# Optimization experiments

Hardware: AMD Instinct MI355X
Metric: run time of the kernel (lower is better)

The kernel has to match this reference:

```python
import jax, jax.numpy as jnp
import numpy as np

N, P = 65536, 1024

def setup_inputs() -> dict:
    key = jax.random.key(0)
    k1, k2, k3, k4 = jax.random.split(key, 4)
    X = jax.random.normal(k1, (N, P), dtype=jnp.float32)
    beta0 = jax.random.normal(k2, (1,), dtype=jnp.float32)
    beta = jax.random.normal(k3, (P,), dtype=jnp.float32)
    Theta = jax.random.normal(k4, (P, P), dtype=jnp.float32)
    return {"X": X, "beta0": beta0, "beta": beta, "Theta": Theta}

def reference(X, beta0, beta, Theta):
    # y_hat = beta0 + X @ beta + sum_{j<k} Theta[j,k] * X[:,j] * X[:,k]
    # The double loop uses only the strictly upper-triangular part of Theta.
    p = Theta.shape[0]
    theta_upper = jnp.triu(Theta, k=1)                     # [p, p]
    linear = beta0 + X @ beta                              # [n]
    interaction = jnp.sum((X @ theta_upper) * X, axis=1)   # [n], quadratic form
    return linear + interaction
```

## Files before the change

### kernel.cpp

```cpp
#include <hip/hip_runtime.h>


typedef __bf16 bf16_t;
typedef bf16_t bf16x8 __attribute__((ext_vector_type(8)));
typedef float f32x4 __attribute__((ext_vector_type(4)));
typedef unsigned short u16;
typedef u16 u16x4 __attribute__((ext_vector_type(4)));
typedef u16 u16x8 __attribute__((ext_vector_type(8)));

#define N_ROWS 65536
#define P_DIM  1024
#define BM 128
#define BN 128
#define BK 32

static __device__ __forceinline__ u16 f2bf(float f) {
  unsigned u = __builtin_bit_cast(unsigned, f);
  u += 0x7FFFu + ((u >> 16) & 1u);
  return (u16)(u >> 16);
}

static __device__ __forceinline__ void gload16(const void* g, void* lds_base) {
  __builtin_amdgcn_global_load_lds(
      (const __attribute__((address_space(1))) unsigned char*)g,
      (__attribute__((address_space(3))) unsigned char*)lds_base, 16, 0, 0);
}

__global__ void __launch_bounds__(256)
init_y(float* __restrict__ y, const float* __restrict__ beta0) {
  int i = blockIdx.x * blockDim.x + threadIdx.x;
  if (i < N_ROWS) y[i] = beta0[0];
}

__global__ void __launch_bounds__(128)
conv_theta(const float* __restrict__ Theta, u16* __restrict__ Tt,
           float* __restrict__ y, const float* __restrict__ beta0) {
  __shared__ float tile[32][33];
  const int tid = threadIdx.x;
  const int tg  = (blockIdx.y * gridDim.x + blockIdx.x) * 128 + tid;
  if (tg < N_ROWS) y[tg] = beta0[0];

  const int k0  = blockIdx.x * 32;
  const int c0  = blockIdx.y * 32;
  {
    const int tx = tid & 31;
    const int rb = tid >> 5;
    #pragma unroll
    for (int i = 0; i < 8; ++i) {
      int kl = rb * 8 + i;
      tile[kl][tx] = Theta[(size_t)(k0 + kl) * P_DIM + c0 + tx];
    }
  }
  __syncthreads();
  {
    const int cl = tid >> 2;
    const int qt = tid & 3;
    const int c  = c0 + cl;
    const int Q  = blockIdx.x * 4 + qt;
    u16x8 w;
    #pragma unroll
    for (int e = 0; e < 8; ++e) {
      int k = Q * 8 + e;
      float v = tile[qt * 8 + e][cl];
      w[e] = (k < c) ? f2bf(v) : (u16)0;
    }
    const int qs = (qt ^ ((c >> 1) & 3));
    *(u16x8*)(Tt + (size_t)c * P_DIM + (size_t)(blockIdx.x * 32 + qs * 8)) = w;
  }
}

__global__ void __launch_bounds__(512)
gemm_r13(const float* __restrict__ X, const u16* __restrict__ Tt,
         const float* __restrict__ beta, float* __restrict__ y)
{
  __shared__ __align__(16) u16 L[2][8192];

  const int nwg = (N_ROWS / BM) * (P_DIM / BN);
  const int swz = (blockIdx.x & 7) * (nwg / 8) + (blockIdx.x >> 3);
  const int bn  = 7 - (swz & 7);
  const int bm  = swz >> 3;
  const int c0  = bn * BN;
  const int m0  = bm * BM;
  const int nkt = (bn + 1) * 4;

  const int tid  = threadIdx.x;
  const int lane = tid & 63;
  const int wid  = tid >> 6;
  const int wm   = wid >> 1;
  const int wn   = wid & 1;
  const int l15  = lane & 15;
  const int lg   = lane >> 4;

  const int ar = tid >> 2;
  const int ap = tid & 3;
  const int aq = (ap ^ ((ar >> 1) & 3)) * 8;

  const int brow = wid * 16 + (lane >> 2);
  const int bq   = (lane & 3) * 8;

  f32x4 acc[2][4];
  #pragma unroll
  for (int i = 0; i < 2; ++i)
    #pragma unroll
    for (int j = 0; j < 4; ++j)
      acc[i][j] = (f32x4)0.0f;

  f32x4 av0, av1;

  #define STAGE_A_LOAD(t_)                                                      \
    {                                                                           \
      const float* s_ = X + (size_t)(m0 + ar) * P_DIM + (t_) * BK + ap * 8;     \
      av0 = ((const f32x4*)s_)[0];                                              \
      av1 = ((const f32x4*)s_)[1];                                              \
    }
  #define STAGE_A_WRITE(buf_)                                                   \
    {                                                                           \
      u16x8 w_;                                                                 \
      _Pragma("unroll")                                                         \
      for (int j = 0; j < 4; ++j) { w_[j] = f2bf(av0[j]); w_[j + 4] = f2bf(av1[j]); } \
      *(u16x8*)&L[buf_][ar * 32 + aq] = w_;                                     \
    }
  #define STAGE_B(buf_, t_)                                                     \
    gload16(Tt + (size_t)(c0 + brow) * P_DIM + (t_) * BK + bq,                  \
            &L[buf_][4096 + wid * 512]);

  STAGE_A_LOAD(0)
  STAGE_B(0, 0)
  asm volatile("s_waitcnt vmcnt(0)" ::: "memory");
  __builtin_amdgcn_sched_barrier(0);
  STAGE_A_WRITE(0)
  asm volatile("s_waitcnt lgkmcnt(0)" ::: "memory");
  __builtin_amdgcn_sched_barrier(0);
  __builtin_amdgcn_s_barrier();
  __builtin_amdgcn_sched_barrier(0);

  for (int t = 0; t < nkt; ++t) {
    const int cur = t & 1;
    const bool pre = (t + 1 < nkt);
    if (pre) { STAGE_A_LOAD(t + 1) STAGE_B(cur ^ 1, t + 1) }

    bf16x8 af[2], bfr[4];
    #pragma unroll
    for (int mi = 0; mi < 2; ++mi) {
      const int rw = wm * 32 + mi * 16 + l15;
      u16x8 v = *(const u16x8*)&L[cur][rw * 32 + (lg ^ ((rw >> 1) & 3)) * 8];
      af[mi] = __builtin_bit_cast(bf16x8, v);
    }
    #pragma unroll
    for (int ni = 0; ni < 4; ++ni) {
      const int cl = wn * 64 + ni * 16 + l15;
      u16x8 v = *(const u16x8*)&L[cur][4096 + cl * 32 + (lg ^ ((cl >> 1) & 3)) * 8];
      bfr[ni] = __builtin_bit_cast(bf16x8, v);
    }

    __builtin_amdgcn_s_setprio(1);
    #pragma unroll
    for (int mi = 0; mi < 2; ++mi)
      #pragma unroll
      for (int ni = 0; ni < 4; ++ni)
        acc[mi][ni] = __builtin_amdgcn_mfma_f32_16x16x32_bf16(bfr[ni], af[mi], acc[mi][ni], 0, 0, 0);
    __builtin_amdgcn_s_setprio(0);

    if (pre) {
      asm volatile("s_waitcnt vmcnt(0)" ::: "memory");
      __builtin_amdgcn_sched_barrier(0);
      STAGE_A_WRITE(cur ^ 1)
    }
    asm volatile("s_waitcnt lgkmcnt(0)" ::: "memory");
    __builtin_amdgcn_sched_barrier(0);
    __builtin_amdgcn_s_barrier();
    __builtin_amdgcn_sched_barrier(0);
  }
  #undef STAGE_A_LOAD
  #undef STAGE_A_WRITE
  #undef STAGE_B

  float ysum[2];
  ysum[0] = 0.0f; ysum[1] = 0.0f;

  #pragma unroll
  for (int mi = 0; mi < 2; ++mi) {
    const int row = m0 + wm * 32 + mi * 16 + l15;
    const float* xr = X + (size_t)row * P_DIM;
    #pragma unroll
    for (int ni = 0; ni < 4; ++ni) {
      const int cb = c0 + wn * 64 + ni * 16 + lg * 4;
      f32x4 xw = *(const f32x4*)(xr + cb);
      f32x4 bv = *(const f32x4*)(beta + cb);
      #pragma unroll
      for (int r = 0; r < 4; ++r)
        ysum[mi] += (acc[mi][ni][r] + bv[r]) * xw[r];
    }
  }

  #pragma unroll
  for (int mi = 0; mi < 2; ++mi) {
    ysum[mi] += __shfl_xor(ysum[mi], 16);
    ysum[mi] += __shfl_xor(ysum[mi], 32);
  }
  if (lane < 16) {
    #pragma unroll
    for (int mi = 0; mi < 2; ++mi)
      atomicAdd(&y[m0 + wm * 32 + mi * 16 + l15], ysum[mi]);
  }
}

#define LDT 40
__global__ void __launch_bounds__(256)
fused_quad_fallback(const float* __restrict__ X, const float* __restrict__ beta,
                    const float* __restrict__ Theta, float* __restrict__ y)
{
  __shared__ __align__(16) u16 Alds[128 * LDT];
  __shared__ __align__(16) u16 Blds[128 * LDT];

  const int bid = blockIdx.x;
  const int bn  = bid & 7;
  const int bm  = bid >> 3;
  const int c0  = bn * 128;
  const int m0  = bm * 128;
  const int nkt = (bn + 1) * 4;

  const int tid  = threadIdx.x;
  const int lane = tid & 63;
  const int wid  = tid >> 6;
  const int wm   = wid >> 1;
  const int wn   = wid & 1;
  const int l15  = lane & 15;
  const int lg   = lane >> 4;

  f32x4 acc[4][4];
  #pragma unroll
  for (int i = 0; i < 4; ++i)
    #pragma unroll
    for (int j = 0; j < 4; ++j)
      acc[i][j] = (f32x4)0.0f;

  const int arow  = tid >> 1;
  const int ahalf = (tid & 1) * 16;
  const int kb4 = (tid >> 5) * 4;
  const int cb4 = (tid & 31) * 4;

  for (int kt = 0; kt < nkt; ++kt) {
    const int k0 = kt * 32;
    __syncthreads();
    {
      const f32x4* p = (const f32x4*)(X + (size_t)(m0 + arow) * P_DIM + k0 + ahalf);
      f32x4 v0 = p[0], v1 = p[1], v2 = p[2], v3 = p[3];
      u16x8 w0, w1;
      #pragma unroll
      for (int i = 0; i < 4; ++i) {
        w0[i] = f2bf(v0[i]); w0[i + 4] = f2bf(v1[i]);
        w1[i] = f2bf(v2[i]); w1[i + 4] = f2bf(v3[i]);
      }
      *(u16x8*)&Alds[arow * LDT + ahalf]     = w0;
      *(u16x8*)&Alds[arow * LDT + ahalf + 8] = w1;
    }
    {
      float e[4][4];
      #pragma unroll
      for (int i = 0; i < 4; ++i) {
        f32x4 r = *(const f32x4*)(Theta + (size_t)(k0 + kb4 + i) * P_DIM + c0 + cb4);
        #pragma unroll
        for (int j = 0; j < 4; ++j)
          e[i][j] = ((k0 + kb4 + i) < (c0 + cb4 + j)) ? r[j] : 0.0f;
      }
      #pragma unroll
      for (int j = 0; j < 4; ++j) {
        u16x4 wv;
        #pragma unroll
        for (int i = 0; i < 4; ++i) wv[i] = f2bf(e[i][j]);
        *(u16x4*)&Blds[(cb4 + j) * LDT + kb4] = wv;
      }
    }
    __syncthreads();

    bf16x8 af[4], bfr[4];
    #pragma unroll
    for (int mi = 0; mi < 4; ++mi) {
      u16x8 t = *(const u16x8*)&Alds[(wm * 64 + mi * 16 + l15) * LDT + lg * 8];
      af[mi] = __builtin_bit_cast(bf16x8, t);
    }
    #pragma unroll
    for (int ni = 0; ni < 4; ++ni) {
      u16x8 t = *(const u16x8*)&Blds[(wn * 64 + ni * 16 + l15) * LDT + lg * 8];
      bfr[ni] = __builtin_bit_cast(bf16x8, t);
    }
    #pragma unroll
    for (int mi = 0; mi < 4; ++mi)
      #pragma unroll
      for (int ni = 0; ni < 4; ++ni)
        acc[mi][ni] = __builtin_amdgcn_mfma_f32_16x16x32_bf16(af[mi], bfr[ni], acc[mi][ni], 0, 0, 0);
  }

  float ysum[4][4];
  #pragma unroll
  for (int mi = 0; mi < 4; ++mi)
    #pragma unroll
    for (int r = 0; r < 4; ++r)
      ysum[mi][r] = 0.0f;

  #pragma unroll
  for (int ni = 0; ni < 4; ++ni) {
    const int col = c0 + wn * 64 + ni * 16 + l15;
    const float bta = beta[col];
    #pragma unroll
    for (int mi = 0; mi < 4; ++mi) {
      const int rowb = m0 + wm * 64 + mi * 16 + lg * 4;
      #pragma unroll
      for (int r = 0; r < 4; ++r) {
        float xv = X[(size_t)(rowb + r) * P_DIM + col];
        ysum[mi][r] += (acc[mi][ni][r] + bta) * xv;
      }
    }
  }

  #pragma unroll
  for (int m = 1; m < 16; m <<= 1)
    #pragma unroll
    for (int mi = 0; mi < 4; ++mi)
      #pragma unroll
      for (int r = 0; r < 4; ++r)
        ysum[mi][r] += __shfl_xor(ysum[mi][r], m);

  if (l15 == 0) {
    #pragma unroll
    for (int mi = 0; mi < 4; ++mi)
      #pragma unroll
      for (int r = 0; r < 4; ++r)
        atomicAdd(&y[m0 + wm * 64 + mi * 16 + lg * 4 + r], ysum[mi][r]);
  }
}

extern "C" void kernel_launch(void* const* d_in, const int* in_sizes, int n_in,
                              void* d_out, int out_size, void* d_ws, size_t ws_size,
                              hipStream_t stream) {
  const float* X     = (const float*)d_in[0];
  const float* beta0 = (const float*)d_in[1];
  const float* beta  = (const float*)d_in[2];
  const float* Theta = (const float*)d_in[3];
  float* y = (float*)d_out;

  const size_t need = (size_t)P_DIM * P_DIM * 2;
  if (ws_size >= need) {
    u16* Tt = (u16*)d_ws;
    conv_theta<<<dim3(32, 32), 128, 0, stream>>>(Theta, Tt, y, beta0);
    gemm_r13<<<(N_ROWS / BM) * (P_DIM / BN), 512, 0, stream>>>(X, Tt, beta, y);
  } else {
    init_y<<<N_ROWS / 256, 256, 0, stream>>>(y, beta0);
    fused_quad_fallback<<<(N_ROWS / 128) * (P_DIM / 128), 256, 0, stream>>>(X, beta, Theta, y);
  }
}
```

Baseline: 163.6 us.

## Triple-buffer Theta tiles to prefetch B two k-steps ahead

Splits LDS into a double buffer for the bf16-converted X tile and a triple buffer for the Theta tile loaded by global_load_lds. Theta tiles are now issued two iterations ahead while X stays one ahead, and the wait becomes vmcnt(2) so the newest B prefetch stays in flight across the barrier. The aim is to hide more global load latency for B. It costs extra LDS per block (40KB versus 32KB), which can reduce occupancy, and it depends on vmcnt ordering being correct.

```diff
diff --git a/kernel.cpp b/kernel.cpp
--- a/kernel.cpp
+++ b/kernel.cpp
@@ -70,10 +70,10 @@
 }
 
 __global__ void __launch_bounds__(512)
-gemm_r13(const float* __restrict__ X, const u16* __restrict__ Tt,
+gemm_r16(const float* __restrict__ X, const u16* __restrict__ Tt,
          const float* __restrict__ beta, float* __restrict__ y)
 {
-  __shared__ __align__(16) u16 L[2][8192];
+  __shared__ __align__(16) u16 L[20480];
 
   const int nwg = (N_ROWS / BM) * (P_DIM / BN);
   const int swz = (blockIdx.x & 7) * (nwg / 8) + (blockIdx.x >> 3);
@@ -113,19 +113,20 @@
       av0 = ((const f32x4*)s_)[0];                                              \
       av1 = ((const f32x4*)s_)[1];                                              \
     }
-  #define STAGE_A_WRITE(buf_)                                                   \
+  #define STAGE_A_WRITE(ab_)                                                    \
     {                                                                           \
       u16x8 w_;                                                                 \
       _Pragma("unroll")                                                         \
       for (int j = 0; j < 4; ++j) { w_[j] = f2bf(av0[j]); w_[j + 4] = f2bf(av1[j]); } \
-      *(u16x8*)&L[buf_][ar * 32 + aq] = w_;                                     \
-    }
-  #define STAGE_B(buf_, t_)                                                     \
+      *(u16x8*)&L[(ab_) * 4096 + ar * 32 + aq] = w_;                            \
+    }
+  #define STAGE_B(bb_, t_)                                                      \
     gload16(Tt + (size_t)(c0 + brow) * P_DIM + (t_) * BK + bq,                  \
-            &L[buf_][4096 + wid * 512]);
-
+            &L[8192 + (bb_) * 4096 + wid * 512]);
+
+  STAGE_B(0, 0)
+  STAGE_B(1, 1)
   STAGE_A_LOAD(0)
-  STAGE_B(0, 0)
   asm volatile("s_waitcnt vmcnt(0)" ::: "memory");
   __builtin_amdgcn_sched_barrier(0);
   STAGE_A_WRITE(0)
@@ -135,21 +136,24 @@
   __builtin_amdgcn_sched_barrier(0);
 
   for (int t = 0; t < nkt; ++t) {
-    const int cur = t & 1;
-    const bool pre = (t + 1 < nkt);
-    if (pre) { STAGE_A_LOAD(t + 1) STAGE_B(cur ^ 1, t + 1) }
+    const int acur = t & 1;
+    const int bcur = t % 3;
+    const bool pre1 = (t + 1 < nkt);
+    const bool pre2 = (t + 2 < nkt);
+    if (pre1) STAGE_A_LOAD(t + 1)
+    if (pre2) STAGE_B((t + 2) % 3, t + 2)
 
     bf16x8 af[2], bfr[4];
     #pragma unroll
     for (int mi = 0; mi < 2; ++mi) {
       const int rw = wm * 32 + mi * 16 + l15;
-      u16x8 v = *(const u16x8*)&L[cur][rw * 32 + (lg ^ ((rw >> 1) & 3)) * 8];
+      u16x8 v = *(const u16x8*)&L[acur * 4096 + rw * 32 + (lg ^ ((rw >> 1) & 3)) * 8];
       af[mi] = __builtin_bit_cast(bf16x8, v);
     }
     #pragma unroll
     for (int ni = 0; ni < 4; ++ni) {
       const int cl = wn * 64 + ni * 16 + l15;
-      u16x8 v = *(const u16x8*)&L[cur][4096 + cl * 32 + (lg ^ ((cl >> 1) & 3)) * 8];
+      u16x8 v = *(const u16x8*)&L[8192 + bcur * 4096 + cl * 32 + (lg ^ ((cl >> 1) & 3)) * 8];
       bfr[ni] = __builtin_bit_cast(bf16x8, v);
     }
 
@@ -161,11 +165,13 @@
         acc[mi][ni] = __builtin_amdgcn_mfma_f32_16x16x32_bf16(bfr[ni], af[mi], acc[mi][ni], 0, 0, 0);
     __builtin_amdgcn_s_setprio(0);
 
-    if (pre) {
+    if (pre2) {
+      asm volatile("s_waitcnt vmcnt(2)" ::: "memory");
+    } else {
       asm volatile("s_waitcnt vmcnt(0)" ::: "memory");
-      __builtin_amdgcn_sched_barrier(0);
-      STAGE_A_WRITE(cur ^ 1)
-    }
+    }
+    __builtin_amdgcn_sched_barrier(0);
+    if (pre1) STAGE_A_WRITE((t + 1) & 1)
     asm volatile("s_waitcnt lgkmcnt(0)" ::: "memory");
     __builtin_amdgcn_sched_barrier(0);
     __builtin_amdgcn_s_barrier();
@@ -344,7 +350,7 @@
   if (ws_size >= need) {
     u16* Tt = (u16*)d_ws;
     conv_theta<<<dim3(32, 32), 128, 0, stream>>>(Theta, Tt, y, beta0);
-    gemm_r13<<<(N_ROWS / BM) * (P_DIM / BN), 512, 0, stream>>>(X, Tt, beta, y);
+    gemm_r16<<<(N_ROWS / BM) * (P_DIM / BN), 512, 0, stream>>>(X, Tt, beta, y);
   } else {
     init_y<<<N_ROWS / 256, 256, 0, stream>>>(y, beta0);
     fused_quad_fallback<<<(N_ROWS / 128) * (P_DIM / 128), 256, 0, stream>>>(X, beta, Theta, y);
```

Measured after the change: 163.0 us. Within noise of the previous version (-0.3%).
